# Performance work log

Measured on AMD Instinct MI355X. Metric: run time of the kernel, lower is better.

The kernel has to match this reference:

```python
import jax, jax.numpy as jnp
import numpy as np

B, S, H = 16, 1024, 768


def setup_inputs() -> dict:
    key = jax.random.key(0)
    ks = jax.random.split(key, 12)
    s = 1.0 / np.sqrt(H)
    return {
        "encoder_outputs": jax.random.normal(ks[0], (B, S, H), dtype=jnp.float32),
        "mask": jax.random.randint(ks[1], (B, S), 0, 2, dtype=jnp.int32),
        "Wq": jax.random.uniform(ks[2], (H, H), jnp.float32, -s, s),
        "bq": jnp.zeros((H,), jnp.float32),
        "Wk": jax.random.uniform(ks[3], (H, H), jnp.float32, -s, s),
        "bk": jnp.zeros((H,), jnp.float32),
        "Wv": jax.random.uniform(ks[4], (H, H), jnp.float32, -s, s),
        "bv": jnp.zeros((H,), jnp.float32),
        "W1": jax.random.uniform(ks[5], (H, H), jnp.float32, -s, s),
        "b1": jnp.zeros((H,), jnp.float32),
        "W2": jax.random.uniform(ks[6], (H, H), jnp.float32, -s, s),
        "b2": jnp.zeros((H,), jnp.float32),
    }


def reference(encoder_outputs, mask, Wq, bq, Wk, bk, Wv, bv, W1, b1, W2, b2):
    x = encoder_outputs  # [B, S, H]
    inv_sqrt_h = 1.0 / jnp.sqrt(jnp.asarray(H, x.dtype))
    # ReLU-gated query/key projections (dropout=0 -> identity)
    q = jax.nn.relu(jnp.einsum('bsh,oh->bso', x, Wq) + bq)
    k = jax.nn.relu(jnp.einsum('bsh,oh->bso', x, Wk) + bk)
    score = jnp.einsum('bsh,bth->bst', q, k) * inv_sqrt_h  # [B, S, S]
    v = jnp.einsum('bsh,oh->bso', x, Wv) + bv
    m = mask.astype(x.dtype)  # [B, S]
    new_mask = m[:, :, None] * m[:, None, :]  # outer product [B, S, S]
    score = score - (1.0 - new_mask) * 1e12
    w = jax.nn.softmax(score, axis=2) * new_mask
    out = jnp.einsum('bst,bth->bsh', w, v)
    # FFN residual
    h1 = jax.nn.relu(jnp.einsum('bsh,oh->bso', out, W1) + b1)
    out = jnp.einsum('bsh,oh->bso', h1, W2) + b2 + out
    return out
```

## Files before the change

### kernel.cpp

```cpp
#include <hip/hip_runtime.h>
#include <hip/hip_bf16.h>

typedef __bf16 bf16_t;
typedef __bf16 bf16x8 __attribute__((ext_vector_type(8)));
typedef __bf16 bf16x4 __attribute__((ext_vector_type(4)));
typedef float f32x4 __attribute__((ext_vector_type(4)));
typedef unsigned int u32;
typedef const __attribute__((address_space(1))) u32* gptr_t;
typedef __attribute__((address_space(3))) u32* lptr_t;

static constexpr int Bb = 16, Ss = 1024, Hh = 768;

__global__ __launch_bounds__(256) void compact_mask(
    const int* __restrict__ mask, int* __restrict__ tok, int* __restrict__ cnt)
{
    const int b = blockIdx.x;
    const int t = threadIdx.x;
    const int4 m4 = *(const int4*)&mask[(b << 10) + (t << 2)];
    const int c = (m4.x != 0) + (m4.y != 0) + (m4.z != 0) + (m4.w != 0);
    __shared__ int sb[256];
    sb[t] = c;
    __syncthreads();
    for (int off = 1; off < 256; off <<= 1) {
        int v = (t >= off) ? sb[t - off] : 0;
        __syncthreads();
        sb[t] += v;
        __syncthreads();
    }
    int p = sb[t] - c;
    int* tb = tok + (b << 10);
    if (m4.x) tb[p++] = (t << 2) + 0;
    if (m4.y) tb[p++] = (t << 2) + 1;
    if (m4.z) tb[p++] = (t << 2) + 2;
    if (m4.w) tb[p++] = (t << 2) + 3;
    if (t == 255) cnt[b] = sb[255];
}

__global__ __launch_bounds__(256) void cvt_all(
    const float* __restrict__ x,
    const float* __restrict__ w0, const float* __restrict__ w1,
    const float* __restrict__ w2, const float* __restrict__ w3,
    const float* __restrict__ w4,
    const float* __restrict__ bq, const float* __restrict__ bk,
    const float* __restrict__ bv,
    const float* __restrict__ b1, const float* __restrict__ b2,
    const int* __restrict__ tok, const int* __restrict__ cnt,
    bf16_t* __restrict__ xc, bf16_t* __restrict__ wdst, float* __restrict__ bdst,
    float* __restrict__ cvec)
{
    const int bx = blockIdx.x;
    const int t = threadIdx.x;
    if (bx < 2880) {
        int seg = bx / 576;
        const float* src = seg == 0 ? w0 : seg == 1 ? w1 : seg == 2 ? w2 : seg == 3 ? w3 : w4;
        int i = (bx % 576) * 256 + t;
        float4 v = ((const float4*)src)[i];
        bf16x4 o = { (bf16_t)v.x, (bf16_t)v.y, (bf16_t)v.z, (bf16_t)v.w };
        ((bf16x4*)(wdst + (long)seg * 589824))[i] = o;
    } else if (bx < 2889) {
        int i = (bx - 2880) * 256 + t;
        if (i < 2304)
            bdst[i] = i < 768 ? bq[i] : i < 1536 ? bk[i - 768] : bv[i - 1536];
    } else if (bx < 19273) {
        const int idx = bx - 2889;
        const int b = idx >> 10, j = idx & 1023;
        if (j < cnt[b] && t < 192) {
            const int s = tok[(b << 10) + j];
            float4 v = ((const float4*)(x + ((long)((b << 10) + s)) * 768))[t];
            bf16x4 o = { (bf16_t)v.x, (bf16_t)v.y, (bf16_t)v.z, (bf16_t)v.w };
            ((bf16x4*)(xc + ((long)((b << 10) + j)) * 768))[t] = o;
        }
    } else {
        const int o = ((bx - 19273) << 3) + (t >> 5);
        const int l = t & 31;
        const float* wr = w4 + (long)o * 768;
        float acc = 0.f;
        for (int h = l; h < 768; h += 32) acc += wr[h] * fmaxf(b1[h], 0.f);
#pragma unroll
        for (int off = 16; off; off >>= 1) acc += __shfl_down(acc, off, 32);
        if (l == 0) cvec[o] = acc + b2[o];
    }
}

__device__ __forceinline__ void async_cp16(const void* g, void* l)
{
    __builtin_amdgcn_global_load_lds((gptr_t)g, (lptr_t)l, 16, 0, 0);
}

enum { EG_QKV = 0, EG_SCORE_C = 1, EG_PV = 2, EG_FFN1 = 3, EG_FFN2 = 4 };

template <int EPI, int BM, int BN>
__global__ __launch_bounds__(256) void mfma_gemm(
    const bf16_t* __restrict__ A, const bf16_t* __restrict__ B,
    const float* __restrict__ bias, const bf16_t* __restrict__ resid,
    const int* __restrict__ tok, const int* __restrict__ cnt,
    void* __restrict__ Cout, bf16_t* __restrict__ out2, bf16_t* __restrict__ out3,
    int K, int lda, int ldb, long sA, long sB, float scale)
{
    const int gx = gridDim.x, gy = gridDim.y;
    const int nwg = gx * gy * gridDim.z;
    int lid = blockIdx.x + gx * (blockIdx.y + gy * blockIdx.z);
    lid = (lid & 7) * (nwg >> 3) + (lid >> 3);
    const int bxs = lid % gx;
    const int tmp = lid / gx;
    const int bys = tmp % gy;
    const int bz  = tmp / gy;

    const int cb = cnt[bz];
    const int m0 = bys * BM;
    const int n0 = bxs * BN;
    if (m0 >= cb) return;
    if constexpr (EPI == EG_SCORE_C) { if (n0 >= cb) return; }
    const int Kend = (EPI == EG_PV) ? ((cb + 31) & ~31) : K;
    const int nk = Kend >> 5;

    constexpr int PM = BM / 2, PN = BN / 2;
    constexpr int MI = PM / 16, NI = PN / 16;
    constexpr int ASZ = BM * 32, BSZ = BN * 32;
    constexpr int NB = 3;

    __shared__ __align__(16) bf16_t Asl[NB * ASZ];
    __shared__ __align__(16) bf16_t Bsl[NB * BSZ];

    const int tid = threadIdx.x;
    const int wid = tid >> 6;
    const int lane = tid & 63;
    const int wm = wid & 1, wn = wid >> 1;

    const bf16_t* Ab = A + (long)bz * sA;
    const bf16_t* Bp = B + (long)bz * sB;

    const int srow = (wid << 4) + (lane >> 2);
    const int scol = ((lane & 3) ^ ((lane >> 3) & 3)) << 3;

    const bf16_t* pa0 = Ab + (long)(m0 + srow) * lda + scol;
    const bf16_t* pa1 = Ab + (long)(m0 + 64 + srow) * lda + scol;
    const bf16_t* pb0 = Bp + (long)(n0 + srow) * ldb + scol;
    const bf16_t* pb1 = Bp + (long)(n0 + 64 + srow) * ldb + scol;

    const int woff = wid << 9;

    const int frag_off = ((lane & 15) << 5) + (((lane >> 4) ^ ((lane >> 1) & 3)) << 3);

    f32x4 acc[MI][NI] = {};

    auto stage = [&](int kk, int buf) {
        bf16_t* la = &Asl[buf * ASZ + woff];
        bf16_t* lb = &Bsl[buf * BSZ + woff];
        async_cp16(pa0 + kk, la);
        if constexpr (BM == 128) async_cp16(pa1 + kk, la + 2048);
        async_cp16(pb0 + kk, lb);
        if constexpr (BN == 128) async_cp16(pb1 + kk, lb + 2048);
    };

    stage(0, 0);
    if (nk > 1) stage(32, 1);
    __builtin_amdgcn_sched_barrier(0);
    if (nk > 1) asm volatile("s_waitcnt vmcnt(4)" ::: "memory");
    else        asm volatile("s_waitcnt vmcnt(0)" ::: "memory");
    __builtin_amdgcn_s_barrier();

    int cur = 0;
    for (int it = 0; it < nk; ++it) {
        if (it + 2 < nk) {
            int tgt = cur + 2; if (tgt >= NB) tgt -= NB;
            stage((it + 2) << 5, tgt);
        }

        const int cba = cur * ASZ, cbb = cur * BSZ;
        bf16x8 af[MI], bfr[NI];
#pragma unroll
        for (int i = 0; i < MI; i++)
            af[i] = *(const bf16x8*)&Asl[cba + ((wm * MI + i) << 9) + frag_off];
#pragma unroll
        for (int j = 0; j < NI; j++)
            bfr[j] = *(const bf16x8*)&Bsl[cbb + ((wn * NI + j) << 9) + frag_off];
#pragma unroll
        for (int i = 0; i < MI; i++)
#pragma unroll
            for (int j = 0; j < NI; j++)
                acc[i][j] = __builtin_amdgcn_mfma_f32_16x16x32_bf16(af[i], bfr[j], acc[i][j], 0, 0, 0);

        __builtin_amdgcn_sched_barrier(0);
        if (it + 1 < nk) {
            if (it + 2 < nk) asm volatile("s_waitcnt vmcnt(4)" ::: "memory");
            else             asm volatile("s_waitcnt vmcnt(0)" ::: "memory");
            __builtin_amdgcn_s_barrier();
        }
        cur = (cur + 1 == NB) ? 0 : cur + 1;
    }

    const int mb_ = m0 + wm * PM;
    const int nb_ = n0 + wn * PN;
    const int colw = lane & 15;
    const int rowq = (lane >> 4) << 2;

    if constexpr (EPI == EG_QKV) {
        float bj[NI];
#pragma unroll
        for (int j = 0; j < NI; j++) bj[j] = bias[nb_ + (j << 4) + colw];
        if (nb_ < 1536) {
            bf16_t* C = ((nb_ < 768) ? (bf16_t*)Cout : out2) + (long)bz * 786432;
            const int cbase = (nb_ < 768) ? nb_ : nb_ - 768;
#pragma unroll
            for (int i = 0; i < MI; i++)
#pragma unroll
                for (int j = 0; j < NI; j++)
#pragma unroll
                    for (int r = 0; r < 4; r++) {
                        int row = mb_ + (i << 4) + rowq + r;
                        int col = cbase + (j << 4) + colw;
                        C[(long)row * Hh + col] = (bf16_t)fmaxf(acc[i][j][r] + bj[j], 0.f);
                    }
        } else {
            bf16_t* C = out3 + (long)bz * 786432;
#pragma unroll
            for (int i = 0; i < MI; i++) {
                const int jc0 = mb_ + (i << 4) + rowq;
#pragma unroll
                for (int j = 0; j < NI; j++) {
                    const int col = nb_ - 1536 + (j << 4) + colw;
                    bf16x4 o = { (bf16_t)(acc[i][j][0] + bj[j]), (bf16_t)(acc[i][j][1] + bj[j]),
                                 (bf16_t)(acc[i][j][2] + bj[j]), (bf16_t)(acc[i][j][3] + bj[j]) };
                    *(bf16x4*)&C[(long)col * 1024 + jc0] = o;
                }
            }
        }
    } else if constexpr (EPI == EG_SCORE_C) {
        bf16_t* C = (bf16_t*)Cout + (long)bz * 1048576;
#pragma unroll
        for (int i = 0; i < MI; i++) {
            const int kbase = mb_ + (i << 4) + rowq;
#pragma unroll
            for (int j = 0; j < NI; j++) {
                const int qrow = nb_ + (j << 4) + colw;
                bf16x4 o = { (bf16_t)(acc[i][j][0] * scale), (bf16_t)(acc[i][j][1] * scale),
                             (bf16_t)(acc[i][j][2] * scale), (bf16_t)(acc[i][j][3] * scale) };
                *(bf16x4*)&C[(long)qrow * 1024 + kbase] = o;
            }
        }
    } else if constexpr (EPI == EG_FFN2) {
        float* outp = (float*)Cout;
        const bf16_t* crow = resid + (long)bz * 786432;
        const int* tb = tok + (bz << 10);
        float bj[NI];
#pragma unroll
        for (int j = 0; j < NI; j++) bj[j] = bias[nb_ + (j << 4) + colw];
#pragma unroll
        for (int i = 0; i < MI; i++)
#pragma unroll
            for (int r = 0; r < 4; r++) {
                const int jq = mb_ + (i << 4) + rowq + r;
                if (jq < cb) {
                    const int s = tb[jq];
                    float* orow = outp + ((long)((bz << 10) + s)) * 768;
                    const bf16_t* cr = crow + (long)jq * 768;
#pragma unroll
                    for (int j = 0; j < NI; j++) {
                        const int col = nb_ + (j << 4) + colw;
                        orow[col] = acc[i][j][r] + bj[j] + (float)cr[col];
                    }
                }
            }
    } else {
        bf16_t* C = (bf16_t*)Cout + (long)bz * 786432;
        float bj[NI];
#pragma unroll
        for (int j = 0; j < NI; j++) bj[j] = 0.f;
        if constexpr (EPI == EG_FFN1) {
#pragma unroll
            for (int j = 0; j < NI; j++) bj[j] = bias[nb_ + (j << 4) + colw];
        }
#pragma unroll
        for (int i = 0; i < MI; i++)
#pragma unroll
            for (int j = 0; j < NI; j++)
#pragma unroll
                for (int r = 0; r < 4; r++) {
                    int row = mb_ + (i << 4) + rowq + r;
                    int col = nb_ + (j << 4) + colw;
                    float v = acc[i][j][r] + bj[j];
                    if constexpr (EPI == EG_FFN1) v = fmaxf(v, 0.f);
                    C[(long)row * Hh + col] = (bf16_t)v;
                }
    }
}

__global__ __launch_bounds__(256) void softmax_rows(
    bf16_t* __restrict__ S_, const int* __restrict__ cnt,
    const int* __restrict__ mask, const float* __restrict__ cvec,
    float* __restrict__ out)
{
    const int b = blockIdx.y;
    const int t = threadIdx.x;

    if (blockIdx.z == 1) {
        const int s = blockIdx.x;
        if (t >= 192 || mask[(b << 10) + s]) return;
        float4 v = ((const float4*)cvec)[t];
        ((float4*)(out + ((long)((b << 10) + s)) * 768))[t] = v;
        return;
    }

    const int jq = blockIdx.x;
    const int cb = cnt[b];
    if (jq >= cb) return;
    bf16_t* p = S_ + (((long)(b << 10)) + jq) * 1024;
    const int t0 = t << 2;

    bf16x4 v4 = *(const bf16x4*)&p[t0];
    float v0 = (t0 + 0 < cb) ? (float)v4[0] : -1e30f;
    float v1 = (t0 + 1 < cb) ? (float)v4[1] : -1e30f;
    float v2 = (t0 + 2 < cb) ? (float)v4[2] : -1e30f;
    float v3 = (t0 + 3 < cb) ? (float)v4[3] : -1e30f;

    float mx = fmaxf(fmaxf(v0, v1), fmaxf(v2, v3));
#pragma unroll
    for (int off = 32; off; off >>= 1) mx = fmaxf(mx, __shfl_down(mx, off, 64));
    __shared__ float redm[4], reds[4];
    if ((t & 63) == 0) redm[t >> 6] = mx;
    __syncthreads();
    mx = fmaxf(fmaxf(redm[0], redm[1]), fmaxf(redm[2], redm[3]));

    float e0 = __expf(v0 - mx), e1 = __expf(v1 - mx);
    float e2 = __expf(v2 - mx), e3 = __expf(v3 - mx);
    float sm = e0 + e1 + e2 + e3;
#pragma unroll
    for (int off = 32; off; off >>= 1) sm += __shfl_down(sm, off, 64);
    if ((t & 63) == 0) reds[t >> 6] = sm;
    __syncthreads();
    sm = reds[0] + reds[1] + reds[2] + reds[3];

    const float inv = 1.f / sm;
    bf16x4 o = { (bf16_t)(e0 * inv), (bf16_t)(e1 * inv),
                 (bf16_t)(e2 * inv), (bf16_t)(e3 * inv) };
    *(bf16x4*)&p[t0] = o;
}

extern "C" void kernel_launch(void* const* d_in, const int* in_sizes, int n_in,
                              void* d_out, int out_size, void* d_ws, size_t ws_size,
                              hipStream_t stream)
{
    const float* x  = (const float*)d_in[0];
    const int* mask = (const int*)d_in[1];
    const float* Wq = (const float*)d_in[2];
    const float* bq = (const float*)d_in[3];
    const float* Wk = (const float*)d_in[4];
    const float* bk = (const float*)d_in[5];
    const float* Wv = (const float*)d_in[6];
    const float* bv = (const float*)d_in[7];
    const float* W1 = (const float*)d_in[8];
    const float* b1 = (const float*)d_in[9];
    const float* W2 = (const float*)d_in[10];
    const float* b2 = (const float*)d_in[11];
    float* out = (float*)d_out;

    char* w = (char*)d_ws;
    bf16_t* xc   = (bf16_t*)(w + 0);
    bf16_t* qc   = (bf16_t*)(w + 25165824);
    bf16_t* kc   = (bf16_t*)(w + 50331648);
    bf16_t* vTc  = (bf16_t*)(w + 75497472);
    bf16_t* sc   = (bf16_t*)(w + 100663296);
    bf16_t* wqkv = (bf16_t*)(w + 134217728);
    bf16_t* w1b  = (bf16_t*)(w + 137756672);
    bf16_t* w2b  = (bf16_t*)(w + 138936320);
    float*  bqkv = (float*) (w + 140115968);
    int*    tok  = (int*)   (w + 140125184);
    int*    cnt  = (int*)   (w + 140190720);
    float*  cvec = (float*) (w + 140190784);
    bf16_t* ctxc = xc;
    bf16_t* h1c  = qc;

    const float inv_sqrt_h = 0.036084391824351615f;
    dim3 blk(256);

    compact_mask<<<16, blk, 0, stream>>>(mask, tok, cnt);
    cvt_all<<<19369, blk, 0, stream>>>(x, Wq, Wk, Wv, W1, W2, bq, bk, bv, b1, b2,
                                       tok, cnt, xc, wqkv, bqkv, cvec);

    mfma_gemm<EG_QKV, 128, 128><<<dim3(18, 8, 16), blk, 0, stream>>>(
        xc, wqkv, bqkv, nullptr, tok, cnt, qc, kc, vTc,
        768, 768, 768, 786432, 0, 1.f);

    mfma_gemm<EG_SCORE_C, 128, 128><<<dim3(8, 8, 16), blk, 0, stream>>>(
        kc, qc, nullptr, nullptr, tok, cnt, sc, nullptr, nullptr,
        768, 768, 768, 786432, 786432, inv_sqrt_h);

    softmax_rows<<<dim3(1024, 16, 2), blk, 0, stream>>>(sc, cnt, mask, cvec, out);

    mfma_gemm<EG_PV, 128, 128><<<dim3(6, 8, 16), blk, 0, stream>>>(
        sc, vTc, nullptr, nullptr, tok, cnt, ctxc, nullptr, nullptr,
        0, 1024, 1024, 1048576, 786432, 1.f);

    mfma_gemm<EG_FFN1, 128, 128><<<dim3(6, 8, 16), blk, 0, stream>>>(
        ctxc, w1b, b1, nullptr, tok, cnt, h1c, nullptr, nullptr,
        768, 768, 768, 786432, 0, 1.f);

    mfma_gemm<EG_FFN2, 128, 128><<<dim3(6, 8, 16), blk, 0, stream>>>(
        h1c, w2b, b2, ctxc, tok, cnt, out, nullptr, nullptr,
        768, 768, 768, 786432, 0, 1.f);
}
```

Baseline: 291.2 us.

## Deepen GEMM LDS pipeline to four stages and double-buffer fragment registers

The MFMA GEMM main loop grows from three to four LDS buffers, so global-to-LDS prefetch runs three k-steps ahead. Fragment loads from LDS now go into two alternating register sets: the fragments for step it+1 are read while the MFMAs for step it run. This is meant to hide global memory latency and LDS read latency behind matrix-core work. In exchange it needs more LDS per block and more VGPRs, which could lower occupancy, and the loop bookkeeping and waitcnt logic become more intricate.

Result: slower. 375.5 us (+29.0%).

```diff
diff --git a/kernel.cpp b/kernel.cpp
--- a/kernel.cpp
+++ b/kernel.cpp
@@ -89,6 +89,9 @@
 
 enum { EG_QKV = 0, EG_SCORE_C = 1, EG_PV = 2, EG_FFN1 = 3, EG_FFN2 = 4 };
 
+#define SBAR __builtin_amdgcn_s_barrier()
+#define VMW(n) asm volatile("s_waitcnt vmcnt(" #n ")" ::: "memory")
+
 template <int EPI, int BM, int BN>
 __global__ __launch_bounds__(256) void mfma_gemm(
     const bf16_t* __restrict__ A, const bf16_t* __restrict__ B,
@@ -117,7 +120,7 @@
     constexpr int PM = BM / 2, PN = BN / 2;
     constexpr int MI = PM / 16, NI = PN / 16;
     constexpr int ASZ = BM * 32, BSZ = BN * 32;
-    constexpr int NB = 3;
+    constexpr int NB = 4;
 
     __shared__ __align__(16) bf16_t Asl[NB * ASZ];
     __shared__ __align__(16) bf16_t Bsl[NB * BSZ];
@@ -141,8 +144,6 @@
     const int woff = wid << 9;
 
     const int frag_off = ((lane & 15) << 5) + (((lane >> 4) ^ ((lane >> 1) & 3)) << 3);
-
-    f32x4 acc[MI][NI] = {};
 
     auto stage = [&](int kk, int buf) {
         bf16_t* la = &Asl[buf * ASZ + woff];
@@ -153,42 +154,45 @@
         if constexpr (BN == 128) async_cp16(pb1 + kk, lb + 2048);
     };
 
+    f32x4 acc[MI][NI] = {};
+    bf16x8 aA[MI], bA[NI], aB[MI], bB[NI];
+
+#define RD_FRAGS(av, bv, buf) do { \
+    const int _ca = (buf) * ASZ, _cb2 = (buf) * BSZ; \
+    _Pragma("unroll") for (int _i = 0; _i < MI; _i++) \
+        av[_i] = *(const bf16x8*)&Asl[_ca + ((wm * MI + _i) << 9) + frag_off]; \
+    _Pragma("unroll") for (int _j = 0; _j < NI; _j++) \
+        bv[_j] = *(const bf16x8*)&Bsl[_cb2 + ((wn * NI + _j) << 9) + frag_off]; } while (0)
+
+#define MFMA_SET(av, bv) do { \
+    _Pragma("unroll") for (int _i = 0; _i < MI; _i++) \
+    _Pragma("unroll") for (int _j = 0; _j < NI; _j++) \
+        acc[_i][_j] = __builtin_amdgcn_mfma_f32_16x16x32_bf16(av[_i], bv[_j], acc[_i][_j], 0, 0, 0); } while (0)
+
     stage(0, 0);
     if (nk > 1) stage(32, 1);
+    if (nk > 2) stage(64, 2);
     __builtin_amdgcn_sched_barrier(0);
-    if (nk > 1) asm volatile("s_waitcnt vmcnt(4)" ::: "memory");
-    else        asm volatile("s_waitcnt vmcnt(0)" ::: "memory");
-    __builtin_amdgcn_s_barrier();
-
-    int cur = 0;
-    for (int it = 0; it < nk; ++it) {
-        if (it + 2 < nk) {
-            int tgt = cur + 2; if (tgt >= NB) tgt -= NB;
-            stage((it + 2) << 5, tgt);
-        }
-
-        const int cba = cur * ASZ, cbb = cur * BSZ;
-        bf16x8 af[MI], bfr[NI];
-#pragma unroll
-        for (int i = 0; i < MI; i++)
-            af[i] = *(const bf16x8*)&Asl[cba + ((wm * MI + i) << 9) + frag_off];
-#pragma unroll
-        for (int j = 0; j < NI; j++)
-            bfr[j] = *(const bf16x8*)&Bsl[cbb + ((wn * NI + j) << 9) + frag_off];
-#pragma unroll
-        for (int i = 0; i < MI; i++)
-#pragma unroll
-            for (int j = 0; j < NI; j++)
-                acc[i][j] = __builtin_amdgcn_mfma_f32_16x16x32_bf16(af[i], bfr[j], acc[i][j], 0, 0, 0);
-
+    if (nk > 2) { VMW(4); } else { VMW(0); }
+    SBAR;
+    RD_FRAGS(aA, bA, 0);
+
+#pragma unroll 2
+    for (int it = 0; it < nk - 1; ++it) {
+        if (it + 3 < nk) stage((it + 3) << 5, (it + 3) & 3);
+        if (it & 1) RD_FRAGS(aA, bA, (it + 1) & 3);
+        else        RD_FRAGS(aB, bB, (it + 1) & 3);
         __builtin_amdgcn_sched_barrier(0);
-        if (it + 1 < nk) {
-            if (it + 2 < nk) asm volatile("s_waitcnt vmcnt(4)" ::: "memory");
-            else             asm volatile("s_waitcnt vmcnt(0)" ::: "memory");
-            __builtin_amdgcn_s_barrier();
-        }
-        cur = (cur + 1 == NB) ? 0 : cur + 1;
+        if (it & 1) MFMA_SET(aB, bB);
+        else        MFMA_SET(aA, bA);
+        __builtin_amdgcn_sched_barrier(0);
+        if (it + 3 < nk) { VMW(4); } else { VMW(0); }
+        SBAR;
     }
+    asm volatile("s_waitcnt lgkmcnt(0)" ::: "memory");
+    __builtin_amdgcn_sched_barrier(0);
+    if (nk & 1) MFMA_SET(aA, bA);
+    else        MFMA_SET(aB, bB);
 
     const int mb_ = m0 + wm * PM;
     const int nb_ = n0 + wn * PN;
@@ -284,6 +288,8 @@
                     C[(long)row * Hh + col] = (bf16_t)v;
                 }
     }
+#undef RD_FRAGS
+#undef MFMA_SET
 }
 
 __global__ __launch_bounds__(256) void softmax_rows(
```
